# Kernel optimization log

Hardware: AMD Instinct MI355X
Metric: run time of the kernel (lower is better)

## Reference

```python
import jax, jax.numpy as jnp
import numpy as np

N = 100_000   # nodes
E = 3_200_000 # edges (avg degree 32)
K = 10        # propagation hops


def setup_inputs() -> dict:
    key = jax.random.key(0)
    ks = jax.random.split(key, 9)
    x = jax.random.normal(ks[0], (N, 1), dtype=jnp.float32)
    edge_index = jax.random.randint(ks[1], (2, E), 0, N, dtype=jnp.int32)
    # MLP params (lin1: 1->32, lin2: 32->64, fc2: 64->1)
    W1 = jax.random.normal(ks[2], (1, 32), dtype=jnp.float32) * 0.5
    b1 = jnp.zeros((32,), dtype=jnp.float32)
    W2 = jax.random.normal(ks[3], (32, 64), dtype=jnp.float32) * (1.0 / np.sqrt(32))
    b2 = jnp.zeros((64,), dtype=jnp.float32)
    # GPR temp coefficients, Init='Random': uniform(-b, b), b=sqrt(3/(K+1)), L1-normalized
    bound = float(np.sqrt(3.0 / (K + 1)))
    temp = jax.random.uniform(ks[4], (K + 1,), dtype=jnp.float32,
                              minval=-bound, maxval=bound)
    temp = temp / jnp.sum(jnp.abs(temp))
    W_fc = jax.random.normal(ks[5], (64, 1), dtype=jnp.float32) * (1.0 / np.sqrt(64))
    b_fc = jnp.zeros((1,), dtype=jnp.float32)
    return {"x": x, "edge_index": edge_index, "W1": W1, "b1": b1,
            "W2": W2, "b2": b2, "temp": temp, "W_fc": W_fc, "b_fc": b_fc}


def reference(x, edge_index, W1, b1, W2, b2, temp, W_fc, b_fc):
    n = x.shape[0]
    # feature MLP
    h = jax.nn.relu(x @ W1 + b1)       # [N, 32]
    h = jax.nn.relu(h @ W2 + b2)       # [N, 64]
    # gcn_norm with self-loops, edge_weight = 1
    loops = jnp.arange(n, dtype=edge_index.dtype)
    row = jnp.concatenate([edge_index[0], loops])  # source
    col = jnp.concatenate([edge_index[1], loops])  # target (aggregation index)
    ones = jnp.ones(row.shape, dtype=h.dtype)
    deg = jax.ops.segment_sum(ones, col, num_segments=n)
    dinv = jnp.where(deg > 0, jax.lax.rsqrt(deg), 0.0)
    norm = dinv[row] * dinv[col]       # [E+N]
    # K-hop GPR propagation: hidden = sum_k temp[k] * A_hat^k h
    hidden0 = temp[0] * h

    def step(carry, gamma):
        xc, hid = carry
        msg = norm[:, None] * xc[row]                       # gather + scale
        xn = jax.ops.segment_sum(msg, col, num_segments=n)  # scatter-add
        return (xn, hid + gamma * xn), None

    (_, hidden), _ = jax.lax.scan(step, (h, hidden0), temp[1:])
    return hidden @ W_fc + b_fc        # [N, 1]
```

## Files before the change

### kernel.cpp

```cpp
#include <hip/hip_runtime.h>


#define TPB 256
#define SBSH 10
#define CAP1 34304
#define CH   16384

__global__ void k_zero(int* __restrict__ bcursor, int nsb) {
    int i = blockIdx.x * blockDim.x + threadIdx.x;
    if (i < nsb) bcursor[i] = 0;
}

__global__ void k_scatter(const int* __restrict__ erow, const int* __restrict__ ecol,
                          int* __restrict__ bcursor, unsigned int* __restrict__ ebuf1,
                          int e, int nsb) {
    __shared__ int hist[128];
    __shared__ int base[128];
    int t = threadIdx.x;
    int s = blockIdx.x * CH;
    int end = min(e, s + CH);

    if (t < 128) hist[t] = 0;
    __syncthreads();
    for (int i = s + t; i < end; i += TPB)
        atomicAdd(&hist[ecol[i] >> SBSH], 1);
    __syncthreads();
    if (t < nsb) {
        int c = hist[t];
        base[t] = c ? atomicAdd(&bcursor[t], c) : 0;
        hist[t] = 0;
    }
    __syncthreads();
    for (int i = s + t; i < end; i += TPB) {
        int c = ecol[i];
        int r = erow[i];
        int b = c >> SBSH;
        int pos = base[b] + atomicAdd(&hist[b], 1);
        if (pos < CAP1)
            ebuf1[(size_t)b * CAP1 + pos] =
                ((unsigned int)r << SBSH) | (unsigned int)(c & ((1 << SBSH) - 1));
    }
}

__global__ void __launch_bounds__(1024)
k_sub(const int* __restrict__ bcursor, const unsigned int* __restrict__ ebuf1,
      unsigned int* __restrict__ csr, int* __restrict__ rs,
      float* __restrict__ dinv, float* __restrict__ dinv2,
      float* __restrict__ sdeg, int n, int e, int nsb) {
    __shared__ int hist[1024];
    __shared__ int hscan[1024];
    __shared__ int hcur[1024];
    __shared__ int sbase;
    int b = blockIdx.x;
    int t = threadIdx.x;

    if (t == 0) {
        int acc = 0;
        for (int i = 0; i < b; i++) acc += min(bcursor[i], CAP1);
        sbase = acc;
    }
    hist[t] = 0;
    __syncthreads();

    int cnt = min(bcursor[b], CAP1);
    size_t g = (size_t)b * CAP1;
    for (int j = t; j < cnt; j += 1024)
        atomicAdd(&hist[ebuf1[g + j] & 1023], 1);
    __syncthreads();

    hscan[t] = hist[t];
    __syncthreads();
    for (int o = 1; o < 1024; o <<= 1) {
        int v = (t >= o) ? hscan[t - o] : 0;
        __syncthreads();
        hscan[t] += v;
        __syncthreads();
    }
    int excl = hscan[t] - hist[t];
    hcur[t] = 0;
    int node = (b << SBSH) + t;
    if (node < n) {
        rs[node] = sbase + excl;
        float d = (float)(hist[t] + 1);
        float di = rsqrtf(d);
        dinv[node] = di;
        dinv2[node] = di * di;
        sdeg[node] = d * di;
    }
    if (b == 0 && t == 0) rs[n] = e;
    __syncthreads();
    hscan[t] = excl;
    __syncthreads();

    for (int j = t; j < cnt; j += 1024) {
        unsigned int p = ebuf1[g + j];
        int sub = p & 1023;
        int pos = sbase + hscan[sub] + atomicAdd(&hcur[sub], 1);
        csr[pos] = p >> SBSH;
    }
}

__global__ void k_mlp_z(const float* __restrict__ x, const float* __restrict__ W1,
                        const float* __restrict__ b1, const float* __restrict__ W2,
                        const float* __restrict__ b2, const float* __restrict__ Wfc,
                        const float* __restrict__ bfc, const float* __restrict__ temp,
                        const float* __restrict__ dinv,
                        float* __restrict__ u0, float* __restrict__ out, int n) {
    int wid = (blockIdx.x * blockDim.x + threadIdx.x) >> 6;
    int lane = threadIdx.x & 63;
    if (wid >= n) return;
    float xv = x[wid];
    float acc = b2[lane];
#pragma unroll
    for (int j = 0; j < 32; j++) {
        float h1 = fmaxf(fmaf(xv, W1[j], b1[j]), 0.f);
        acc = fmaf(h1, W2[j * 64 + lane], acc);
    }
    float h2 = fmaxf(acc, 0.f);
    float c = h2 * Wfc[lane];
#pragma unroll
    for (int o = 32; o >= 1; o >>= 1) c += __shfl_xor(c, o);
    if (lane == 0) {
        u0[wid] = dinv[wid] * c;
        out[wid] = fmaf(temp[0], c, bfc[0]);
    }
}

__global__ void k_hop(const int* __restrict__ rs, const unsigned int* __restrict__ csr,
                      const float* __restrict__ dinv2, const float* __restrict__ sdeg,
                      const float* __restrict__ uprev, float* __restrict__ ucur,
                      float* __restrict__ out, const float* __restrict__ temp,
                      int k, int n) {
    int tid = blockIdx.x * blockDim.x + threadIdx.x;
    int node = tid >> 2;
    int sub = tid & 3;
    if (node >= n) return;
    int s = rs[node];
    int epos = rs[node + 1];
    float sum = (sub == 0) ? uprev[node] : 0.f;
    for (int i = s + sub; i < epos; i += 4)
        sum += uprev[csr[i]];
    sum += __shfl_xor(sum, 1);
    sum += __shfl_xor(sum, 2);
    if (sub == 0) {
        float u = dinv2[node] * sum;
        ucur[node] = u;
        out[node] = fmaf(temp[k] * sdeg[node], u, out[node]);
    }
}

static inline size_t align256(size_t x) { return (x + 255) & ~(size_t)255; }

extern "C" void kernel_launch(void* const* d_in, const int* in_sizes, int n_in,
                              void* d_out, int out_size, void* d_ws, size_t ws_size,
                              hipStream_t stream) {
    const float* x    = (const float*)d_in[0];
    const int*   ei   = (const int*)d_in[1];
    const float* W1   = (const float*)d_in[2];
    const float* b1   = (const float*)d_in[3];
    const float* W2   = (const float*)d_in[4];
    const float* b2   = (const float*)d_in[5];
    const float* temp = (const float*)d_in[6];
    const float* Wfc  = (const float*)d_in[7];
    const float* bfc  = (const float*)d_in[8];

    const int n = in_sizes[0];
    const int e = in_sizes[1] / 2;
    const int K = in_sizes[6] - 1;
    const int nsb = (n + (1 << SBSH) - 1) >> SBSH;

    const int* erow = ei;
    const int* ecol = ei + e;

    float* out = (float*)d_out;

    char* ws = (char*)d_ws;
    int*          bcursor = (int*)ws;          ws += align256((size_t)128 * 4);
    unsigned int* ebuf1   = (unsigned int*)ws; ws += align256((size_t)nsb * CAP1 * 4);
    unsigned int* csr     = (unsigned int*)ws; ws += align256((size_t)e * 4);
    int*          rs      = (int*)ws;          ws += align256((size_t)(n + 1) * 4);
    float*        dinv    = (float*)ws;        ws += align256((size_t)n * 4);
    float*        dinv2   = (float*)ws;        ws += align256((size_t)n * 4);
    float*        sdeg    = (float*)ws;        ws += align256((size_t)n * 4);
    float*        u0      = (float*)ws;        ws += align256((size_t)n * 4);
    float*        u1      = (float*)ws;        ws += align256((size_t)n * 4);

    const int gS = (e + CH - 1) / CH;
    const int gW = (n + 3) / 4;
    const int gH = (4 * n + TPB - 1) / TPB;

    k_zero<<<1, 128, 0, stream>>>(bcursor, nsb);
    k_scatter<<<gS, TPB, 0, stream>>>(erow, ecol, bcursor, ebuf1, e, nsb);
    k_sub<<<nsb, 1024, 0, stream>>>(bcursor, ebuf1, csr, rs, dinv, dinv2, sdeg, n, e, nsb);
    k_mlp_z<<<gW, 256, 0, stream>>>(x, W1, b1, W2, b2, Wfc, bfc, temp, dinv, u0, out, n);

    float* uin = u0;
    float* uout = u1;
    for (int k = 1; k <= K; k++) {
        k_hop<<<gH, TPB, 0, stream>>>(rs, csr, dinv2, sdeg, uin, uout, out, temp, k, n);
        float* t2 = uin; uin = uout; uout = t2;
    }
}
```

Measured before the change: 403.3 us.

## Drop serial prefix in CSR build, use padded CSR with per-node end, 8 lanes/node

The scatter kernel now loads its 16 edges per thread into registers once and reuses them for both histogram passes, replacing the second global read. The sub-bucket kernel drops the serial per-block prefix over earlier buckets and the barrier-heavy 1024-step scan, using a wave-shuffle scan instead. It writes CSR into a padded per-bucket layout with separate start and end arrays. The hop kernel uses 8 lanes per node instead of 4. The costs are a larger CSR workspace, an extra end-index array read per node, and more idle lanes for low-degree nodes.

Result: faster. 360.7 us (-10.6%).

```diff
diff --git a/kernel.cpp b/kernel.cpp
--- a/kernel.cpp
+++ b/kernel.cpp
@@ -1,10 +1,11 @@
 #include <hip/hip_runtime.h>
 
 
-#define TPB 256
+#define TPB  256
 #define SBSH 10
 #define CAP1 34304
-#define CH   16384
+#define EPT  16
+#define CH   (TPB * EPT)
 
 __global__ void k_zero(int* __restrict__ bcursor, int nsb) {
     int i = blockIdx.x * blockDim.x + threadIdx.x;
@@ -18,85 +19,97 @@
     __shared__ int base[128];
     int t = threadIdx.x;
     int s = blockIdx.x * CH;
-    int end = min(e, s + CH);
+    int r[EPT], c[EPT];
 
     if (t < 128) hist[t] = 0;
     __syncthreads();
-    for (int i = s + t; i < end; i += TPB)
-        atomicAdd(&hist[ecol[i] >> SBSH], 1);
+#pragma unroll
+    for (int j = 0; j < EPT; j++) {
+        int i = s + j * TPB + t;
+        bool ok = (i < e);
+        c[j] = ok ? ecol[i] : -1;
+        r[j] = ok ? erow[i] : 0;
+        if (ok) atomicAdd(&hist[c[j] >> SBSH], 1);
+    }
     __syncthreads();
     if (t < nsb) {
-        int c = hist[t];
-        base[t] = c ? atomicAdd(&bcursor[t], c) : 0;
+        int cc = hist[t];
+        base[t] = cc ? atomicAdd(&bcursor[t], cc) : 0;
         hist[t] = 0;
     }
     __syncthreads();
-    for (int i = s + t; i < end; i += TPB) {
-        int c = ecol[i];
-        int r = erow[i];
-        int b = c >> SBSH;
-        int pos = base[b] + atomicAdd(&hist[b], 1);
-        if (pos < CAP1)
-            ebuf1[(size_t)b * CAP1 + pos] =
-                ((unsigned int)r << SBSH) | (unsigned int)(c & ((1 << SBSH) - 1));
+#pragma unroll
+    for (int j = 0; j < EPT; j++) {
+        if (c[j] >= 0) {
+            int b = c[j] >> SBSH;
+            int pos = base[b] + atomicAdd(&hist[b], 1);
+            if (pos < CAP1)
+                ebuf1[(size_t)b * CAP1 + pos] =
+                    ((unsigned int)r[j] << SBSH) | (unsigned int)(c[j] & ((1 << SBSH) - 1));
+        }
     }
 }
 
 __global__ void __launch_bounds__(1024)
 k_sub(const int* __restrict__ bcursor, const unsigned int* __restrict__ ebuf1,
-      unsigned int* __restrict__ csr, int* __restrict__ rs,
+      unsigned int* __restrict__ csr, int* __restrict__ rs, int* __restrict__ re,
       float* __restrict__ dinv, float* __restrict__ dinv2,
-      float* __restrict__ sdeg, int n, int e, int nsb) {
+      float* __restrict__ sdeg, int n) {
     __shared__ int hist[1024];
-    __shared__ int hscan[1024];
-    __shared__ int hcur[1024];
-    __shared__ int sbase;
+    __shared__ int wsum[16];
     int b = blockIdx.x;
     int t = threadIdx.x;
-
-    if (t == 0) {
-        int acc = 0;
-        for (int i = 0; i < b; i++) acc += min(bcursor[i], CAP1);
-        sbase = acc;
-    }
+    int lane = t & 63;
+    int w = t >> 6;
+
     hist[t] = 0;
     __syncthreads();
-
     int cnt = min(bcursor[b], CAP1);
     size_t g = (size_t)b * CAP1;
     for (int j = t; j < cnt; j += 1024)
         atomicAdd(&hist[ebuf1[g + j] & 1023], 1);
     __syncthreads();
 
-    hscan[t] = hist[t];
-    __syncthreads();
-    for (int o = 1; o < 1024; o <<= 1) {
-        int v = (t >= o) ? hscan[t - o] : 0;
-        __syncthreads();
-        hscan[t] += v;
-        __syncthreads();
-    }
-    int excl = hscan[t] - hist[t];
-    hcur[t] = 0;
+    int deg = hist[t];
+    int v = deg;
+#pragma unroll
+    for (int o = 1; o < 64; o <<= 1) {
+        int u = __shfl_up(v, o);
+        if (lane >= o) v += u;
+    }
+    if (lane == 63) wsum[w] = v;
+    __syncthreads();
+    if (w == 0) {
+        int sv = (lane < 16) ? wsum[lane] : 0;
+#pragma unroll
+        for (int o = 1; o < 16; o <<= 1) {
+            int u = __shfl_up(sv, o);
+            if (lane >= o) sv += u;
+        }
+        if (lane < 16) wsum[lane] = sv;
+    }
+    __syncthreads();
+    int excl = v - deg + (w > 0 ? wsum[w - 1] : 0);
+
     int node = (b << SBSH) + t;
     if (node < n) {
-        rs[node] = sbase + excl;
-        float d = (float)(hist[t] + 1);
+        int base = (int)g + excl;
+        rs[node] = base;
+        re[node] = base + deg;
+        float d = (float)(deg + 1);
         float di = rsqrtf(d);
         dinv[node] = di;
         dinv2[node] = di * di;
         sdeg[node] = d * di;
     }
-    if (b == 0 && t == 0) rs[n] = e;
-    __syncthreads();
-    hscan[t] = excl;
-    __syncthreads();
-
+    __syncthreads();
+    hist[t] = excl;
+    __syncthreads();
     for (int j = t; j < cnt; j += 1024) {
         unsigned int p = ebuf1[g + j];
         int sub = p & 1023;
-        int pos = sbase + hscan[sub] + atomicAdd(&hcur[sub], 1);
-        csr[pos] = p >> SBSH;
+        int pos = atomicAdd(&hist[sub], 1);
+        csr[g + pos] = p >> SBSH;
     }
 }
 
@@ -126,22 +139,24 @@
     }
 }
 
-__global__ void k_hop(const int* __restrict__ rs, const unsigned int* __restrict__ csr,
+__global__ void k_hop(const int* __restrict__ rs, const int* __restrict__ re,
+                      const unsigned int* __restrict__ csr,
                       const float* __restrict__ dinv2, const float* __restrict__ sdeg,
                       const float* __restrict__ uprev, float* __restrict__ ucur,
                       float* __restrict__ out, const float* __restrict__ temp,
                       int k, int n) {
     int tid = blockIdx.x * blockDim.x + threadIdx.x;
-    int node = tid >> 2;
-    int sub = tid & 3;
+    int node = tid >> 3;
+    int sub = tid & 7;
     if (node >= n) return;
     int s = rs[node];
-    int epos = rs[node + 1];
+    int epos = re[node];
     float sum = (sub == 0) ? uprev[node] : 0.f;
-    for (int i = s + sub; i < epos; i += 4)
+    for (int i = s + sub; i < epos; i += 8)
         sum += uprev[csr[i]];
     sum += __shfl_xor(sum, 1);
     sum += __shfl_xor(sum, 2);
+    sum += __shfl_xor(sum, 4);
     if (sub == 0) {
         float u = dinv2[node] * sum;
         ucur[node] = u;
@@ -177,8 +192,9 @@
     char* ws = (char*)d_ws;
     int*          bcursor = (int*)ws;          ws += align256((size_t)128 * 4);
     unsigned int* ebuf1   = (unsigned int*)ws; ws += align256((size_t)nsb * CAP1 * 4);
-    unsigned int* csr     = (unsigned int*)ws; ws += align256((size_t)e * 4);
-    int*          rs      = (int*)ws;          ws += align256((size_t)(n + 1) * 4);
+    unsigned int* csr     = (unsigned int*)ws; ws += align256((size_t)nsb * CAP1 * 4);
+    int*          rs      = (int*)ws;          ws += align256((size_t)n * 4);
+    int*          re      = (int*)ws;          ws += align256((size_t)n * 4);
     float*        dinv    = (float*)ws;        ws += align256((size_t)n * 4);
     float*        dinv2   = (float*)ws;        ws += align256((size_t)n * 4);
     float*        sdeg    = (float*)ws;        ws += align256((size_t)n * 4);
@@ -187,17 +203,17 @@
 
     const int gS = (e + CH - 1) / CH;
     const int gW = (n + 3) / 4;
-    const int gH = (4 * n + TPB - 1) / TPB;
+    const int gH = (8 * n + TPB - 1) / TPB;
 
     k_zero<<<1, 128, 0, stream>>>(bcursor, nsb);
     k_scatter<<<gS, TPB, 0, stream>>>(erow, ecol, bcursor, ebuf1, e, nsb);
-    k_sub<<<nsb, 1024, 0, stream>>>(bcursor, ebuf1, csr, rs, dinv, dinv2, sdeg, n, e, nsb);
+    k_sub<<<nsb, 1024, 0, stream>>>(bcursor, ebuf1, csr, rs, re, dinv, dinv2, sdeg, n);
     k_mlp_z<<<gW, 256, 0, stream>>>(x, W1, b1, W2, b2, Wfc, bfc, temp, dinv, u0, out, n);
 
     float* uin = u0;
     float* uout = u1;
     for (int k = 1; k <= K; k++) {
-        k_hop<<<gH, TPB, 0, stream>>>(rs, csr, dinv2, sdeg, uin, uout, out, temp, k, n);
+        k_hop<<<gH, TPB, 0, stream>>>(rs, re, csr, dinv2, sdeg, uin, uout, out, temp, k, n);
         float* t2 = uin; uin = uout; uout = t2;
     }
 }
```
